# Kernel optimization log

Hardware: AMD Instinct MI355X
Metric: run time of the kernel (lower is better)

The kernel has to match this reference:

```python
import jax, jax.numpy as jnp
import numpy as np

N = 4
IN_F = 4096
OUT_F = 4096
TOKENS = 8192


def setup_inputs() -> dict:
    key = jax.random.key(0)
    k1, k2, k3, k4 = jax.random.split(key, 4)
    x = jax.random.normal(k1, (TOKENS, IN_F), dtype=jnp.float32)
    a = jax.random.normal(k2, (N, N, N), dtype=jnp.float32) * 0.1
    s = jax.random.normal(k3, (N, OUT_F // N, IN_F // N), dtype=jnp.float32) * 0.02
    bias = jax.random.normal(k4, (OUT_F,), dtype=jnp.float32) * 0.01
    return {"x": x, "a": a, "s": s, "bias": bias}


def reference(x, a, s, bias):
    # weight = sum_k kron(a[k], s[k]); kron block (i,j) scaled s[k].
    # w[i*P+p, j*Q+q] = sum_k a[k,i,j] * s[k,p,q]
    n = a.shape[0]
    P, Q = s.shape[1], s.shape[2]
    w = jnp.einsum('kij,kpq->ipjq', a, s).reshape(n * P, n * Q)  # [out, in]
    return x @ w.T + bias
```

## Files before the change

kernel.cpp:

```cpp
#include <hip/hip_runtime.h>
#include <hip/hip_bf16.h>

#define TOKENS 8192
#define IN_F   4096
#define OUT_F  4096
#define GK     IN_F
#define GN     OUT_F

#define BM 128
#define BN 128
#define BK 64

typedef __attribute__((ext_vector_type(8))) short bf16x8;
typedef __attribute__((ext_vector_type(4))) float f32x4;
typedef __attribute__((address_space(1))) void gvoid;
typedef __attribute__((address_space(3))) void lvoid;

static __device__ __forceinline__ unsigned short f32_to_bf16(float f) {
  union { float f; unsigned int u; } v; v.f = f;
  unsigned int u = v.u;
  return (unsigned short)((u + 0x7FFFu + ((u >> 16) & 1u)) >> 16);
}

__global__ void cast_x_kernel(const float4* __restrict__ x, bf16x8* __restrict__ xb) {
  int idx = blockIdx.x * blockDim.x + threadIdx.x;
  float4 v0 = x[idx * 2];
  float4 v1 = x[idx * 2 + 1];
  bf16x8 r;
  r[0] = (short)f32_to_bf16(v0.x); r[1] = (short)f32_to_bf16(v0.y);
  r[2] = (short)f32_to_bf16(v0.z); r[3] = (short)f32_to_bf16(v0.w);
  r[4] = (short)f32_to_bf16(v1.x); r[5] = (short)f32_to_bf16(v1.y);
  r[6] = (short)f32_to_bf16(v1.z); r[7] = (short)f32_to_bf16(v1.w);
  xb[idx] = r;
}

__global__ void build_w_kernel(const float* __restrict__ a, const float* __restrict__ s,
                               unsigned short* __restrict__ wb) {
  int gid = blockIdx.x * blockDim.x + threadIdx.x;
  int o = gid >> 10;
  int i = (gid & 1023) << 2;
  int ib = o >> 10, p = o & 1023;
  int jb = i >> 10, q = i & 1023;
  float r0 = 0.f, r1 = 0.f, r2 = 0.f, r3 = 0.f;
#pragma unroll
  for (int k = 0; k < 4; ++k) {
    float ak = a[k * 16 + ib * 4 + jb];
    const float4 sv = *(const float4*)(s + (((size_t)(k * 1024 + p)) << 10) + q);
    r0 += ak * sv.x; r1 += ak * sv.y; r2 += ak * sv.z; r3 += ak * sv.w;
  }
  ushort4 w;
  w.x = f32_to_bf16(r0); w.y = f32_to_bf16(r1);
  w.z = f32_to_bf16(r2); w.w = f32_to_bf16(r3);
  *(ushort4*)(wb + ((size_t)o << 12) + i) = w;
}

__global__ __launch_bounds__(256, 2)
void gemm_bias_kernel(const unsigned short* __restrict__ A,
                      const unsigned short* __restrict__ B,
                      const float* __restrict__ bias,
                      float* __restrict__ C) {
  __shared__ unsigned short As[BM * BK];
  __shared__ unsigned short Bs[BN * BK];

  const int tid  = threadIdx.x;
  const int lane = tid & 63;
  const int wave = tid >> 6;
  const int m0 = blockIdx.y * BM;
  const int n0 = blockIdx.x * BN;
  const int wm = (wave >> 1) * 64;
  const int wn = (wave & 1) * 64;

  f32x4 acc[4][4];
#pragma unroll
  for (int mi = 0; mi < 4; ++mi)
#pragma unroll
    for (int ni = 0; ni < 4; ++ni)
      acc[mi][ni] = (f32x4){0.f, 0.f, 0.f, 0.f};

  const int srow = tid >> 3;
  const int sgr  = (tid & 7) ^ (srow & 7);
  const unsigned short* Ag = A + (size_t)(m0 + srow) * GK + sgr * 8;
  const unsigned short* Bg = B + (size_t)(n0 + srow) * GK + sgr * 8;
  unsigned short* Asd = As + tid * 8;
  unsigned short* Bsd = Bs + tid * 8;

  const int ln15 = lane & 15;
  const int quad = lane >> 4;
  const int sw   = lane & 7;
  int rowA[4], rowB[4];
#pragma unroll
  for (int t = 0; t < 4; ++t) {
    rowA[t] = (wm + t * 16 + ln15) * BK;
    rowB[t] = (wn + t * 16 + ln15) * BK;
  }

  for (int k0 = 0; k0 < GK; k0 += BK) {
#pragma unroll
    for (int p = 0; p < 4; ++p) {
      __builtin_amdgcn_global_load_lds((const gvoid*)(Ag + (size_t)(p * 32) * GK + k0),
                                       (lvoid*)(Asd + p * 2048), 16, 0, 0);
      __builtin_amdgcn_global_load_lds((const gvoid*)(Bg + (size_t)(p * 32) * GK + k0),
                                       (lvoid*)(Bsd + p * 2048), 16, 0, 0);
    }
    __syncthreads();
#pragma unroll
    for (int half = 0; half < 2; ++half) {
      const int gk   = half * 4 + quad;
      const int cofs = ((gk ^ sw) << 3);
      bf16x8 af[4], bfr[4];
#pragma unroll
      for (int t = 0; t < 4; ++t) {
        af[t]  = *(const bf16x8*)(As + rowA[t] + cofs);
        bfr[t] = *(const bf16x8*)(Bs + rowB[t] + cofs);
      }
#pragma unroll
      for (int mi = 0; mi < 4; ++mi)
#pragma unroll
        for (int ni = 0; ni < 4; ++ni)
          acc[mi][ni] = __builtin_amdgcn_mfma_f32_16x16x32_bf16(af[mi], bfr[ni],
                                                                acc[mi][ni], 0, 0, 0);
    }
    __syncthreads();
  }

#pragma unroll
  for (int ni = 0; ni < 4; ++ni) {
    const int col = n0 + wn + ni * 16 + ln15;
    const float bv = bias[col];
#pragma unroll
    for (int mi = 0; mi < 4; ++mi) {
      const int rowb = m0 + wm + mi * 16 + quad * 4;
#pragma unroll
      for (int r = 0; r < 4; ++r)
        C[(size_t)(rowb + r) * GN + col] = acc[mi][ni][r] + bv;
    }
  }
}

__global__ void naive_kernel(const float* __restrict__ x, const float* __restrict__ a,
                             const float* __restrict__ s, const float* __restrict__ bias,
                             float* __restrict__ out) {
  long long idx = (long long)blockIdx.x * blockDim.x + threadIdx.x;
  if (idx >= (long long)TOKENS * OUT_F) return;
  int t = (int)(idx >> 12);
  int o = (int)(idx & 4095);
  int ib = o >> 10, p = o & 1023;
  float acc = bias[o];
  for (int jb = 0; jb < 4; ++jb) {
    float a0 = a[0  + ib * 4 + jb];
    float a1 = a[16 + ib * 4 + jb];
    float a2 = a[32 + ib * 4 + jb];
    float a3 = a[48 + ib * 4 + jb];
    const float* xr = x + (size_t)t * IN_F + jb * 1024;
    const float* s0 = s + (size_t)p * 1024;
    const float* s1 = s0 + 1048576;
    const float* s2 = s1 + 1048576;
    const float* s3 = s2 + 1048576;
    for (int q = 0; q < 1024; ++q) {
      float w = a0 * s0[q] + a1 * s1[q] + a2 * s2[q] + a3 * s3[q];
      acc += xr[q] * w;
    }
  }
  out[idx] = acc;
}

extern "C" void kernel_launch(void* const* d_in, const int* in_sizes, int n_in,
                              void* d_out, int out_size, void* d_ws, size_t ws_size,
                              hipStream_t stream) {
  const float* x    = (const float*)d_in[0];
  const float* a    = (const float*)d_in[1];
  const float* s    = (const float*)d_in[2];
  const float* bias = (const float*)d_in[3];
  float* out = (float*)d_out;

  const size_t xb_elems = (size_t)TOKENS * IN_F;
  const size_t wb_elems = (size_t)OUT_F * IN_F;
  const size_t need = (xb_elems + wb_elems) * sizeof(unsigned short);

  if (ws_size >= need) {
    unsigned short* Xb = (unsigned short*)d_ws;
    unsigned short* Wb = Xb + xb_elems;
    cast_x_kernel<<<(int)(xb_elems / 8 / 256), 256, 0, stream>>>((const float4*)x, (bf16x8*)Xb);
    build_w_kernel<<<(int)(wb_elems / 4 / 256), 256, 0, stream>>>(a, s, Wb);
    dim3 grid(GN / BN, TOKENS / BM);
    gemm_bias_kernel<<<grid, 256, 0, stream>>>(Xb, Wb, bias, out);
  } else {
    long long total = (long long)TOKENS * OUT_F;
    naive_kernel<<<(int)((total + 255) / 256), 256, 0, stream>>>(x, a, s, bias, out);
  }
}
```

Baseline: 509.1 us.

## Use 256x256 double-buffered GEMM tiles with 8 waves and merge prep kernels

```diff
diff --git a/kernel.cpp b/kernel.cpp
--- a/kernel.cpp
+++ b/kernel.cpp
@@ -1,5 +1,4 @@
 #include <hip/hip_runtime.h>
-#include <hip/hip_bf16.h>
 
 #define TOKENS 8192
 #define IN_F   4096
@@ -7,9 +6,10 @@
 #define GK     IN_F
 #define GN     OUT_F
 
-#define BM 128
-#define BN 128
+#define BM 256
+#define BN 256
 #define BK 64
+#define NT (GK / BK)
 
 typedef __attribute__((ext_vector_type(8))) short bf16x8;
 typedef __attribute__((ext_vector_type(4))) float f32x4;
@@ -22,119 +22,180 @@
   return (unsigned short)((u + 0x7FFFu + ((u >> 16) & 1u)) >> 16);
 }
 
-__global__ void cast_x_kernel(const float4* __restrict__ x, bf16x8* __restrict__ xb) {
-  int idx = blockIdx.x * blockDim.x + threadIdx.x;
-  float4 v0 = x[idx * 2];
-  float4 v1 = x[idx * 2 + 1];
-  bf16x8 r;
-  r[0] = (short)f32_to_bf16(v0.x); r[1] = (short)f32_to_bf16(v0.y);
-  r[2] = (short)f32_to_bf16(v0.z); r[3] = (short)f32_to_bf16(v0.w);
-  r[4] = (short)f32_to_bf16(v1.x); r[5] = (short)f32_to_bf16(v1.y);
-  r[6] = (short)f32_to_bf16(v1.z); r[7] = (short)f32_to_bf16(v1.w);
-  xb[idx] = r;
-}
-
-__global__ void build_w_kernel(const float* __restrict__ a, const float* __restrict__ s,
-                               unsigned short* __restrict__ wb) {
-  int gid = blockIdx.x * blockDim.x + threadIdx.x;
-  int o = gid >> 10;
-  int i = (gid & 1023) << 2;
-  int ib = o >> 10, p = o & 1023;
-  int jb = i >> 10, q = i & 1023;
-  float r0 = 0.f, r1 = 0.f, r2 = 0.f, r3 = 0.f;
-#pragma unroll
-  for (int k = 0; k < 4; ++k) {
-    float ak = a[k * 16 + ib * 4 + jb];
-    const float4 sv = *(const float4*)(s + (((size_t)(k * 1024 + p)) << 10) + q);
-    r0 += ak * sv.x; r1 += ak * sv.y; r2 += ak * sv.z; r3 += ak * sv.w;
-  }
-  ushort4 w;
-  w.x = f32_to_bf16(r0); w.y = f32_to_bf16(r1);
-  w.z = f32_to_bf16(r2); w.w = f32_to_bf16(r3);
-  *(ushort4*)(wb + ((size_t)o << 12) + i) = w;
-}
-
-__global__ __launch_bounds__(256, 2)
+__global__ void prep_kernel(const float4* __restrict__ x, bf16x8* __restrict__ xb,
+                            const float* __restrict__ a, const float* __restrict__ s,
+                            unsigned short* __restrict__ wb) {
+  const int bid = blockIdx.x;
+  if (bid < 16384) {
+    const int idx = bid * 256 + threadIdx.x;
+    float4 v0 = x[idx * 2];
+    float4 v1 = x[idx * 2 + 1];
+    bf16x8 r;
+    r[0] = (short)f32_to_bf16(v0.x); r[1] = (short)f32_to_bf16(v0.y);
+    r[2] = (short)f32_to_bf16(v0.z); r[3] = (short)f32_to_bf16(v0.w);
+    r[4] = (short)f32_to_bf16(v1.x); r[5] = (short)f32_to_bf16(v1.y);
+    r[6] = (short)f32_to_bf16(v1.z); r[7] = (short)f32_to_bf16(v1.w);
+    xb[idx] = r;
+  } else {
+    const int gid = (bid - 16384) * 256 + threadIdx.x;
+    const int o = gid >> 10;
+    const int i = (gid & 1023) << 2;
+    const int ib = o >> 10, p = o & 1023;
+    const int jb = i >> 10, q = i & 1023;
+    float r0 = 0.f, r1 = 0.f, r2 = 0.f, r3 = 0.f;
+#pragma unroll
+    for (int k = 0; k < 4; ++k) {
+      float ak = a[k * 16 + ib * 4 + jb];
+      const float4 sv = *(const float4*)(s + (((size_t)(k * 1024 + p)) << 10) + q);
+      r0 += ak * sv.x; r1 += ak * sv.y; r2 += ak * sv.z; r3 += ak * sv.w;
+    }
+    ushort4 w;
+    w.x = f32_to_bf16(r0); w.y = f32_to_bf16(r1);
+    w.z = f32_to_bf16(r2); w.w = f32_to_bf16(r3);
+    *(ushort4*)(wb + ((size_t)o << 12) + i) = w;
+  }
+}
+
+#define BARRIER() do { __builtin_amdgcn_s_barrier(); asm volatile("" ::: "memory"); } while (0)
+
+__global__ __launch_bounds__(512, 2)
 void gemm_bias_kernel(const unsigned short* __restrict__ A,
                       const unsigned short* __restrict__ B,
                       const float* __restrict__ bias,
                       float* __restrict__ C) {
-  __shared__ unsigned short As[BM * BK];
-  __shared__ unsigned short Bs[BN * BK];
+  __shared__ unsigned short As[2][BM * BK];
+  __shared__ unsigned short Bs[2][BN * BK];
 
   const int tid  = threadIdx.x;
   const int lane = tid & 63;
   const int wave = tid >> 6;
+  const int wr   = wave >> 2;
+  const int wc   = wave & 3;
   const int m0 = blockIdx.y * BM;
   const int n0 = blockIdx.x * BN;
-  const int wm = (wave >> 1) * 64;
-  const int wn = (wave & 1) * 64;
-
-  f32x4 acc[4][4];
-#pragma unroll
-  for (int mi = 0; mi < 4; ++mi)
-#pragma unroll
-    for (int ni = 0; ni < 4; ++ni)
-      acc[mi][ni] = (f32x4){0.f, 0.f, 0.f, 0.f};
+
+  const int ln15 = lane & 15;
+  const int quad = lane >> 4;
+  const int sw   = ln15 & 7;
+  int ck[2];
+  ck[0] = ((0 + quad) ^ sw) << 3;
+  ck[1] = ((4 + quad) ^ sw) << 3;
+
+  unsigned short* Asb = &As[0][0];
+  unsigned short* Bsb = &Bs[0][0];
 
   const int srow = tid >> 3;
   const int sgr  = (tid & 7) ^ (srow & 7);
   const unsigned short* Ag = A + (size_t)(m0 + srow) * GK + sgr * 8;
   const unsigned short* Bg = B + (size_t)(n0 + srow) * GK + sgr * 8;
-  unsigned short* Asd = As + tid * 8;
-  unsigned short* Bsd = Bs + tid * 8;
-
-  const int ln15 = lane & 15;
-  const int quad = lane >> 4;
-  const int sw   = lane & 7;
-  int rowA[4], rowB[4];
-#pragma unroll
-  for (int t = 0; t < 4; ++t) {
-    rowA[t] = (wm + t * 16 + ln15) * BK;
-    rowB[t] = (wn + t * 16 + ln15) * BK;
-  }
-
-  for (int k0 = 0; k0 < GK; k0 += BK) {
-#pragma unroll
-    for (int p = 0; p < 4; ++p) {
-      __builtin_amdgcn_global_load_lds((const gvoid*)(Ag + (size_t)(p * 32) * GK + k0),
-                                       (lvoid*)(Asd + p * 2048), 16, 0, 0);
-      __builtin_amdgcn_global_load_lds((const gvoid*)(Bg + (size_t)(p * 32) * GK + k0),
-                                       (lvoid*)(Bsd + p * 2048), 16, 0, 0);
-    }
-    __syncthreads();
-#pragma unroll
-    for (int half = 0; half < 2; ++half) {
-      const int gk   = half * 4 + quad;
-      const int cofs = ((gk ^ sw) << 3);
-      bf16x8 af[4], bfr[4];
-#pragma unroll
-      for (int t = 0; t < 4; ++t) {
-        af[t]  = *(const bf16x8*)(As + rowA[t] + cofs);
-        bfr[t] = *(const bf16x8*)(Bs + rowB[t] + cofs);
-      }
-#pragma unroll
-      for (int mi = 0; mi < 4; ++mi)
-#pragma unroll
-        for (int ni = 0; ni < 4; ++ni)
-          acc[mi][ni] = __builtin_amdgcn_mfma_f32_16x16x32_bf16(af[mi], bfr[ni],
-                                                                acc[mi][ni], 0, 0, 0);
-    }
-    __syncthreads();
+
+#define STAGE_A(par, h, u) do { \
+    const unsigned short* s_ = Ag + (size_t)((h) * 128) * GK + (u) * BK; \
+    unsigned short* d_ = Asb + (par) * 16384 + (h) * 8192 + tid * 8; \
+    __builtin_amdgcn_global_load_lds((const gvoid*)s_, (lvoid*)d_, 16, 0, 0); \
+    __builtin_amdgcn_global_load_lds((const gvoid*)(s_ + (size_t)64 * GK), (lvoid*)(d_ + 4096), 16, 0, 0); \
+  } while (0)
+
+#define STAGE_B(par, h, u) do { \
+    const unsigned short* s_ = Bg + (size_t)((h) * 128) * GK + (u) * BK; \
+    unsigned short* d_ = Bsb + (par) * 16384 + (h) * 8192 + tid * 8; \
+    __builtin_amdgcn_global_load_lds((const gvoid*)s_, (lvoid*)d_, 16, 0, 0); \
+    __builtin_amdgcn_global_load_lds((const gvoid*)(s_ + (size_t)64 * GK), (lvoid*)(d_ + 4096), 16, 0, 0); \
+  } while (0)
+
+  f32x4 acc[8][4];
+#pragma unroll
+  for (int mi = 0; mi < 8; ++mi)
+#pragma unroll
+    for (int ni = 0; ni < 4; ++ni)
+      acc[mi][ni] = (f32x4){0.f, 0.f, 0.f, 0.f};
+
+  const int aBase = wr * 8192 + ln15 * 64;
+  const int bBase = (wc >> 1) * 8192 + ((wc & 1) * 64 + ln15) * 64;
+
+  bf16x8 bfr[4][2];
+
+  STAGE_B(0, 0, 0); STAGE_B(0, 1, 0);
+  STAGE_A(0, 0, 0); STAGE_A(0, 1, 0);
+  STAGE_B(1, 0, 1); STAGE_B(1, 1, 1);
+
+  for (int t = 0; t < NT; ++t) {
+    const int p  = t & 1;
+    const int u1 = (t + 1 < NT) ? t + 1 : NT - 1;
+    const int u2 = (t + 2 < NT) ? t + 2 : NT - 1;
+    const unsigned short* Ard = Asb + p * 16384 + aBase;
+    const unsigned short* Brd = Bsb + p * 16384 + bBase;
+
+    STAGE_A(p ^ 1, 0, u1);
+    asm volatile("s_waitcnt vmcnt(6)" ::: "memory");
+    BARRIER();
+    {
+      bf16x8 af[2][2];
+#pragma unroll
+      for (int ni = 0; ni < 4; ++ni)
+#pragma unroll
+        for (int kk = 0; kk < 2; ++kk)
+          bfr[ni][kk] = *(const bf16x8*)(Brd + ni * 1024 + ck[kk]);
+#pragma unroll
+      for (int mi2 = 0; mi2 < 2; ++mi2)
+#pragma unroll
+        for (int kk = 0; kk < 2; ++kk)
+          af[mi2][kk] = *(const bf16x8*)(Ard + mi2 * 1024 + ck[kk]);
+      asm volatile("s_waitcnt lgkmcnt(0)" ::: "memory");
+      __builtin_amdgcn_s_setprio(1);
+#pragma unroll
+      for (int kk = 0; kk < 2; ++kk)
+#pragma unroll
+        for (int mi2 = 0; mi2 < 2; ++mi2)
+#pragma unroll
+          for (int ni = 0; ni < 4; ++ni)
+            acc[mi2][ni] = __builtin_amdgcn_mfma_f32_16x16x32_bf16(af[mi2][kk], bfr[ni][kk],
+                                                                   acc[mi2][ni], 0, 0, 0);
+      __builtin_amdgcn_s_setprio(0);
+      BARRIER();
+    }
+
+#pragma unroll
+    for (int q = 1; q < 4; ++q) {
+      bf16x8 af[2][2];
+#pragma unroll
+      for (int mi2 = 0; mi2 < 2; ++mi2)
+#pragma unroll
+        for (int kk = 0; kk < 2; ++kk)
+          af[mi2][kk] = *(const bf16x8*)(Ard + (2 * q + mi2) * 1024 + ck[kk]);
+      if (q == 1)      STAGE_A(p ^ 1, 1, u1);
+      else if (q == 2) STAGE_B(p, 0, u2);
+      else             STAGE_B(p, 1, u2);
+      BARRIER();
+      asm volatile("s_waitcnt lgkmcnt(0)" ::: "memory");
+      __builtin_amdgcn_s_setprio(1);
+#pragma unroll
+      for (int kk = 0; kk < 2; ++kk)
+#pragma unroll
+        for (int mi2 = 0; mi2 < 2; ++mi2)
+#pragma unroll
+          for (int ni = 0; ni < 4; ++ni)
+            acc[2 * q + mi2][ni] = __builtin_amdgcn_mfma_f32_16x16x32_bf16(af[mi2][kk], bfr[ni][kk],
+                                                                           acc[2 * q + mi2][ni], 0, 0, 0);
+      __builtin_amdgcn_s_setprio(0);
+      BARRIER();
+    }
   }
 
 #pragma unroll
   for (int ni = 0; ni < 4; ++ni) {
-    const int col = n0 + wn + ni * 16 + ln15;
+    const int col = n0 + wc * 64 + ni * 16 + ln15;
     const float bv = bias[col];
 #pragma unroll
-    for (int mi = 0; mi < 4; ++mi) {
-      const int rowb = m0 + wm + mi * 16 + quad * 4;
+    for (int mi = 0; mi < 8; ++mi) {
+      const int rowb = m0 + wr * 128 + mi * 16 + quad * 4;
 #pragma unroll
       for (int r = 0; r < 4; ++r)
         C[(size_t)(rowb + r) * GN + col] = acc[mi][ni][r] + bv;
     }
   }
+#undef STAGE_A
+#undef STAGE_B
 }
 
 __global__ void naive_kernel(const float* __restrict__ x, const float* __restrict__ a,
@@ -180,10 +241,12 @@
   if (ws_size >= need) {
     unsigned short* Xb = (unsigned short*)d_ws;
     unsigned short* Wb = Xb + xb_elems;
-    cast_x_kernel<<<(int)(xb_elems / 8 / 256), 256, 0, stream>>>((const float4*)x, (bf16x8*)Xb);
-    build_w_kernel<<<(int)(wb_elems / 4 / 256), 256, 0, stream>>>(a, s, Wb);
+    const int cast_blocks  = (int)(xb_elems / 8 / 256);
+    const int build_blocks = (int)(wb_elems / 4 / 256);
+    prep_kernel<<<cast_blocks + build_blocks, 256, 0, stream>>>(
+        (const float4*)x, (bf16x8*)Xb, a, s, Wb);
     dim3 grid(GN / BN, TOKENS / BM);
-    gemm_bias_kernel<<<grid, 256, 0, stream>>>(Xb, Wb, bias, out);
+    gemm_bias_kernel<<<grid, 512, 0, stream>>>(Xb, Wb, bias, out);
   } else {
     long long total = (long long)TOKENS * OUT_F;
     naive_kernel<<<(int)((total + 255) / 256), 256, 0, stream>>>(x, a, s, bias, out);
```

After: 616.4 us. +21.1%, slower.
